# Performance work log

Hardware: AMD Instinct MI355X
Metric: run time of the kernel (lower is better)

## Reference

```python
import jax, jax.numpy as jnp
import numpy as np

N, CIN, COUT, T, V, K = 32, 64, 64, 1024, 25, 3
EPS = 1e-5  # BatchNorm2d default eps


def setup_inputs() -> dict:
    key = jax.random.key(0)
    ks = jax.random.split(key, 7)
    x = jax.random.normal(ks[0], (N, CIN, T, V), jnp.float32)
    W = jax.random.normal(ks[1], (K * COUT, CIN), jnp.float32) * 0.05  # 1x1 conv weight (squeezed)
    b = jax.random.normal(ks[2], (K * COUT,), jnp.float32) * 0.01
    A = jax.random.uniform(ks[3], (K, V, V), jnp.float32) * 0.1       # fixed adjacency buffer
    PA = jax.random.normal(ks[4], (K, V, V), jnp.float32) * 0.01      # learned adjacency offset
    gamma = jnp.ones((COUT,), jnp.float32)
    beta = jnp.zeros((COUT,), jnp.float32)
    return {"x": x, "W": W, "b": b, "A": A, "PA": PA, "gamma": gamma, "beta": beta}


def reference(x, W, b, A, PA, gamma, beta):
    n, c, t, v = x.shape
    # 1x1 conv: [n,c,t,v] x [K*COUT, c] -> [n, K*COUT, t, v]
    y = jnp.einsum('nctv,oc->notv', x, W) + b[None, :, None, None]
    y = y.reshape(n, K, COUT, t, v)
    Afull = A + PA
    # multi-subset spatial graph aggregation over joints v -> w
    agg = jnp.einsum('nkctv,kvw->nctw', y, Afull)
    # BatchNorm2d (training mode: biased batch stats over N,T,V per channel)
    mu = jnp.mean(agg, axis=(0, 2, 3), keepdims=True)
    var = jnp.var(agg, axis=(0, 2, 3), keepdims=True)
    normed = gamma[None, :, None, None] * (agg - mu) * jax.lax.rsqrt(var + EPS) + beta[None, :, None, None]
    # residual is Identity (in_channels == out_channels), then ReLU
    return jax.nn.relu(normed + x)
```

## Files before the change

### kernel.cpp

```cpp
#include <hip/hip_runtime.h>

#define N_    32
#define CIN_  64
#define COUT_ 64
#define T_    1024
#define V_    25
#define K_    3
#define TT_   4
#define EPSV  1e-5f

#define WS_BIAS2  2112
#define WS_SUM    9856
#define WS_SQ     10368
#define WS_SCALE  10880
#define WS_SHIFT  10944
#define WS_A2F    11008
#define WS_W2F    12288

typedef __attribute__((ext_vector_type(4))) float f32x4;
typedef __attribute__((ext_vector_type(8))) short short8;

__device__ __forceinline__ unsigned short f_to_bf16u(float f) {
    unsigned int b = __float_as_uint(f);
    b += 0x7fffu + ((b >> 16) & 1u);
    return (unsigned short)(b >> 16);
}

__global__ void gcn_prep(const float* __restrict__ A, const float* __restrict__ PA,
                         const float* __restrict__ b, const float* __restrict__ W,
                         float* ws) {
    __shared__ float cs[K_ * V_];
    const int tid = threadIdx.x;
    const int blk = blockIdx.x;

    if (blk == 0) {
        if (tid < K_ * V_) {
            int k = tid / V_, w = tid % V_;
            float s = 0.f;
            for (int v = 0; v < V_; ++v) {
                int idx = (k * V_ + v) * V_ + w;
                s += A[idx] + PA[idx];
            }
            cs[tid] = s;
        }
        for (int f = tid; f < 1024; f += 256) ws[WS_SUM + f] = 0.f;
        __syncthreads();
        for (int f = tid; f < COUT_ * V_; f += 256) {
            int c = f / V_, w = f - (f / V_) * V_;
            float s = 0.f;
            for (int k = 0; k < K_; ++k) s += b[k * COUT_ + c] * cs[k * V_ + w];
            ws[WS_BIAS2 + f] = s;
        }
    } else if (blk == 1) {
        unsigned short* a2 = (unsigned short*)(ws + WS_A2F);
        for (int f = tid; f < 5 * 64 * 8; f += 256) {
            int j  = f & 7;
            int l  = (f >> 3) & 63;
            int nt = f >> 9;
            int col = nt * 16 + (l & 15);
            int v   = (l >> 4) * 8 + j;
            float val = 0.f;
            if (col < 75 && v < V_) {
                int k = col / 25, w = col - (col / 25) * 25;
                int idx = (k * V_ + v) * V_ + w;
                val = A[idx] + PA[idx];
            }
            a2[f] = f_to_bf16u(val);
        }
    } else {
        unsigned short* w2 = (unsigned short*)(ws + WS_W2F);
        int lo = (blk - 2) * 6144;
        for (int f = lo + tid; f < lo + 6144; f += 256) {
            int j = f & 7;
            int l = (f >> 3) & 63;
            int g = f >> 9;
            int kci = (g % 6) * 32 + (l >> 4) * 8 + j;
            int c   = (g / 6) * 16 + (l & 15);
            int k = kci >> 6, ci = kci & 63;
            w2[f] = f_to_bf16u(W[(k * 64 + c) * 64 + ci]);
        }
    }
}

__global__ __launch_bounds__(256, 2)
void gcn_main(const float* __restrict__ x, float* __restrict__ ws,
              float* __restrict__ out) {
    __shared__ __align__(16) unsigned char smem[65280];
    unsigned short* xs16 = (unsigned short*)smem;
    unsigned short* xa16 = (unsigned short*)(smem + 20480);
    float* ostage = (float*)smem;
    float* sstat  = (float*)(smem + 25856);

    const int tid = threadIdx.x;
    const int bid = blockIdx.x;
    const int n   = bid >> 8;
    const int tc  = bid & 255;
    const int l   = tid & 63;
    const int wv  = tid >> 6;
    const int llo = l & 15;
    const int lhi = l >> 4;

    {
        unsigned int* xu = (unsigned int*)xs16;
        #pragma unroll
        for (int i = 0; i < 20; ++i) xu[i * 256 + tid] = 0u;
    }
    __syncthreads();

    const float4* xg = (const float4*)x;
    for (int f = tid; f < CIN_ * 25; f += 256) {
        int ci = f / 25;
        int j  = f - ci * 25;
        float4 g = xg[((size_t)(n * CIN_ + ci)) * 6400 + tc * 25 + j];
        int flat = 4 * j;
        int t = flat / 25;
        int v = flat - t * 25;
        float vals[4] = {g.x, g.y, g.z, g.w};
        #pragma unroll
        for (int e = 0; e < 4; ++e) {
            xs16[(ci * 4 + t) * 40 + v] = f_to_bf16u(vals[e]);
            if (++v == 25) { v = 0; ++t; }
        }
    }
    __syncthreads();

    {
        const unsigned short* a2g = (const unsigned short*)(ws + WS_A2F);
        short8 a2f[5];
        #pragma unroll
        for (int nt = 0; nt < 5; ++nt)
            a2f[nt] = *(const short8*)(a2g + (nt * 64 + l) * 8);

        #pragma unroll
        for (int q = 0; q < 4; ++q) {
            int mt = wv * 4 + q;
            short8 xf = *(const short8*)(xs16 + (mt * 16 + llo) * 40 + lhi * 8);
            f32x4 acc[5];
            #pragma unroll
            for (int nt = 0; nt < 5; ++nt) {
                f32x4 z = {0.f, 0.f, 0.f, 0.f};
                acc[nt] = __builtin_amdgcn_mfma_f32_16x16x32_bf16(xf, a2f[nt], z, 0, 0, 0);
            }
            int ci = mt * 4 + lhi;
            #pragma unroll
            for (int nt = 0; nt < 5; ++nt) {
                int col = nt * 16 + llo;
                if (col < 75) {
                    int k = (col >= 50) ? 2 : ((col >= 25) ? 1 : 0);
                    int w = col - k * 25;
                    unsigned short* dst = xa16 + w * 200 + k * 64 + ci;
                    #pragma unroll
                    for (int i = 0; i < 4; ++i)
                        dst[i * 5000] = f_to_bf16u(acc[nt][i]);
                }
            }
        }
    }
    __syncthreads();

    f32x4 c2[7];
    {
        const unsigned short* w2g = (const unsigned short*)(ws + WS_W2F);
        short8 w2f[6];
        #pragma unroll
        for (int kk = 0; kk < 6; ++kk)
            w2f[kk] = *(const short8*)(w2g + ((wv * 6 + kk) * 64 + l) * 8);

        const int c = wv * 16 + llo;
        #pragma unroll
        for (int mt = 0; mt < 7; ++mt) {
            f32x4 acc = {0.f, 0.f, 0.f, 0.f};
            #pragma unroll
            for (int kk = 0; kk < 6; ++kk) {
                short8 a = *(const short8*)(xa16 + (mt * 16 + llo) * 200 + kk * 32 + lhi * 8);
                acc = __builtin_amdgcn_mfma_f32_16x16x32_bf16(a, w2f[kk], acc, 0, 0, 0);
            }
            int rb = mt * 16 + lhi * 4;
            #pragma unroll
            for (int i = 0; i < 4; ++i) {
                int row2 = rb + i;
                if (row2 < 100) {
                    int t2 = row2 / 25;
                    int w2i = row2 - t2 * 25;
                    acc[i] += ws[WS_BIAS2 + c * 25 + w2i];
                }
            }
            c2[mt] = acc;
        }
    }
    __syncthreads();

    {
        const int c = wv * 16 + llo;
        #pragma unroll
        for (int mt = 0; mt < 7; ++mt) {
            int rb = mt * 16 + lhi * 4;
            #pragma unroll
            for (int i = 0; i < 4; ++i)
                if (rb + i < 100) ostage[c * 101 + rb + i] = c2[mt][i];
        }
    }
    __syncthreads();

    const size_t obase = ((size_t)(n * COUT_)) * 25600 + tc * 100;
    #pragma unroll 1
    for (int it = 0; it < 25; ++it) {
        int idx = it * 256 + tid;
        int cc = idx / 100;
        int r  = idx - cc * 100;
        out[obase + (size_t)cc * 25600 + r] = ostage[cc * 101 + r];
    }

    {
        int cc = tid & 63, tg = tid >> 6;
        float ls = 0.f, lq = 0.f;
        #pragma unroll
        for (int w = 0; w < 25; ++w) {
            float v = ostage[cc * 101 + tg * 25 + w];
            ls += v; lq = fmaf(v, v, lq);
        }
        sstat[(tg * 64 + cc) * 2]     = ls;
        sstat[(tg * 64 + cc) * 2 + 1] = lq;
    }
    __syncthreads();
    if (tid < 64) {
        int cc = tid;
        float s = sstat[cc * 2] + sstat[(64 + cc) * 2] + sstat[(128 + cc) * 2] + sstat[(192 + cc) * 2];
        float q = sstat[cc * 2 + 1] + sstat[(64 + cc) * 2 + 1] + sstat[(128 + cc) * 2 + 1] + sstat[(192 + cc) * 2 + 1];
        int slot = bid & 7;
        atomicAdd(&ws[WS_SUM + slot * 64 + cc], s);
        atomicAdd(&ws[WS_SQ  + slot * 64 + cc], q);
    }
}

__global__ void gcn_stats(float* ws, const float* __restrict__ gamma,
                          const float* __restrict__ beta) {
    int c = threadIdx.x;
    if (c < COUT_) {
        float s = 0.f, q = 0.f;
        #pragma unroll
        for (int slot = 0; slot < 8; ++slot) {
            s += ws[WS_SUM + slot * 64 + c];
            q += ws[WS_SQ  + slot * 64 + c];
        }
        const float cnt = (float)(N_ * T_ * V_);
        float mu  = s / cnt;
        float var = q / cnt - mu * mu;
        float rs  = rsqrtf(var + EPSV);
        float sc  = gamma[c] * rs;
        ws[WS_SCALE + c] = sc;
        ws[WS_SHIFT + c] = fmaf(-mu, sc, beta[c]);
    }
}

__global__ __launch_bounds__(256)
void gcn_finish(const float* __restrict__ x, const float* __restrict__ ws,
                float* __restrict__ out) {
    int bid = blockIdx.x;
    int c = bid & 63;
    float sc = ws[WS_SCALE + c];
    float sh = ws[WS_SHIFT + c];
    size_t base4 = (size_t)bid * 6400;
    const float4* x4 = (const float4*)x;
    float4* o4 = (float4*)out;
    #pragma unroll 2
    for (int it = 0; it < 25; ++it) {
        size_t i = base4 + it * 256 + threadIdx.x;
        float4 a  = o4[i];
        float4 xv = x4[i];
        a.x = fmaxf(0.f, fmaf(a.x, sc, sh) + xv.x);
        a.y = fmaxf(0.f, fmaf(a.y, sc, sh) + xv.y);
        a.z = fmaxf(0.f, fmaf(a.z, sc, sh) + xv.z);
        a.w = fmaxf(0.f, fmaf(a.w, sc, sh) + xv.w);
        o4[i] = a;
    }
}

extern "C" void kernel_launch(void* const* d_in, const int* in_sizes, int n_in,
                              void* d_out, int out_size, void* d_ws, size_t ws_size,
                              hipStream_t stream) {
    (void)in_sizes; (void)n_in; (void)out_size; (void)ws_size;
    const float* x     = (const float*)d_in[0];
    const float* W     = (const float*)d_in[1];
    const float* b     = (const float*)d_in[2];
    const float* A     = (const float*)d_in[3];
    const float* PA    = (const float*)d_in[4];
    const float* gamma = (const float*)d_in[5];
    const float* beta  = (const float*)d_in[6];
    float* out = (float*)d_out;
    float* ws  = (float*)d_ws;

    gcn_prep<<<4, 256, 0, stream>>>(A, PA, b, W, ws);
    gcn_main<<<N_ * (T_ / TT_), 256, 0, stream>>>(x, ws, out);
    gcn_stats<<<1, 64, 0, stream>>>(ws, gamma, beta);
    gcn_finish<<<N_ * COUT_, 256, 0, stream>>>(x, ws, out);
}
```

Before: 641.8 us.

## Halve time tile, drop LDS output staging, store and reduce stats from registers

Each block now handles 2 time steps instead of 4, which doubles the block count, cuts LDS from about 64KB to 35KB and raises launch bounds to 4 blocks per SM. The LDS staging of the output tile and the separate stats pass are removed. Outputs are written straight from MFMA accumulators to global memory, and per-channel sums are reduced with wave shuffles before the atomics. The first-stage results are packed as bf16 pairs into 8-byte LDS stores. The tradeoffs are less coalesced direct global writes, each lane storing strided rows, and twice as many atomics.

```diff
diff --git a/kernel.cpp b/kernel.cpp
--- a/kernel.cpp
+++ b/kernel.cpp
@@ -6,7 +6,7 @@
 #define T_    1024
 #define V_    25
 #define K_    3
-#define TT_   4
+#define TT_   2
 #define EPSV  1e-5f
 
 #define WS_BIAS2  2112
@@ -82,19 +82,17 @@
     }
 }
 
-__global__ __launch_bounds__(256, 2)
+__global__ __launch_bounds__(256, 4)
 void gcn_main(const float* __restrict__ x, float* __restrict__ ws,
               float* __restrict__ out) {
-    __shared__ __align__(16) unsigned char smem[65280];
+    __shared__ __align__(16) unsigned char smem[35840];
     unsigned short* xs16 = (unsigned short*)smem;
-    unsigned short* xa16 = (unsigned short*)(smem + 20480);
-    float* ostage = (float*)smem;
-    float* sstat  = (float*)(smem + 25856);
+    unsigned short* xa16 = (unsigned short*)(smem + 10240);
 
     const int tid = threadIdx.x;
     const int bid = blockIdx.x;
-    const int n   = bid >> 8;
-    const int tc  = bid & 255;
+    const int n   = bid >> 9;
+    const int tc  = bid & 511;
     const int l   = tid & 63;
     const int wv  = tid >> 6;
     const int llo = l & 15;
@@ -103,24 +101,22 @@
     {
         unsigned int* xu = (unsigned int*)xs16;
         #pragma unroll
-        for (int i = 0; i < 20; ++i) xu[i * 256 + tid] = 0u;
+        for (int i = 0; i < 10; ++i) xu[i * 256 + tid] = 0u;
     }
     __syncthreads();
 
-    const float4* xg = (const float4*)x;
+    const float2* xg = (const float2*)x;
     for (int f = tid; f < CIN_ * 25; f += 256) {
         int ci = f / 25;
         int j  = f - ci * 25;
-        float4 g = xg[((size_t)(n * CIN_ + ci)) * 6400 + tc * 25 + j];
-        int flat = 4 * j;
-        int t = flat / 25;
-        int v = flat - t * 25;
-        float vals[4] = {g.x, g.y, g.z, g.w};
-        #pragma unroll
-        for (int e = 0; e < 4; ++e) {
-            xs16[(ci * 4 + t) * 40 + v] = f_to_bf16u(vals[e]);
-            if (++v == 25) { v = 0; ++t; }
-        }
+        float2 g = xg[(size_t)(n * CIN_ + ci) * 12800 + tc * 25 + j];
+        int flat = 2 * j;
+        int t = (flat >= 25) ? 1 : 0;
+        int v = flat - 25 * t;
+        xs16[(t * 64 + ci) * 40 + v] = f_to_bf16u(g.x);
+        int v2 = v + 1, t2 = t;
+        if (v2 == 25) { v2 = 0; t2 = 1; }
+        xs16[(t2 * 64 + ci) * 40 + v2] = f_to_bf16u(g.y);
     }
     __syncthreads();
 
@@ -132,33 +128,32 @@
             a2f[nt] = *(const short8*)(a2g + (nt * 64 + l) * 8);
 
         #pragma unroll
-        for (int q = 0; q < 4; ++q) {
-            int mt = wv * 4 + q;
+        for (int q = 0; q < 2; ++q) {
+            int mt = wv * 2 + q;
             short8 xf = *(const short8*)(xs16 + (mt * 16 + llo) * 40 + lhi * 8);
-            f32x4 acc[5];
+            int rb = mt * 16 + lhi * 4;
+            int t  = rb >> 6;
+            int ci = rb & 63;
             #pragma unroll
             for (int nt = 0; nt < 5; ++nt) {
                 f32x4 z = {0.f, 0.f, 0.f, 0.f};
-                acc[nt] = __builtin_amdgcn_mfma_f32_16x16x32_bf16(xf, a2f[nt], z, 0, 0, 0);
-            }
-            int ci = mt * 4 + lhi;
-            #pragma unroll
-            for (int nt = 0; nt < 5; ++nt) {
+                f32x4 acc = __builtin_amdgcn_mfma_f32_16x16x32_bf16(xf, a2f[nt], z, 0, 0, 0);
                 int col = nt * 16 + llo;
                 if (col < 75) {
                     int k = (col >= 50) ? 2 : ((col >= 25) ? 1 : 0);
                     int w = col - k * 25;
-                    unsigned short* dst = xa16 + w * 200 + k * 64 + ci;
-                    #pragma unroll
-                    for (int i = 0; i < 4; ++i)
-                        dst[i * 5000] = f_to_bf16u(acc[nt][i]);
+                    unsigned int lo = (unsigned int)f_to_bf16u(acc[0]) |
+                                      ((unsigned int)f_to_bf16u(acc[1]) << 16);
+                    unsigned int hi = (unsigned int)f_to_bf16u(acc[2]) |
+                                      ((unsigned int)f_to_bf16u(acc[3]) << 16);
+                    uint2 pk; pk.x = lo; pk.y = hi;
+                    *(uint2*)(xa16 + (t * 25 + w) * 200 + k * 64 + ci) = pk;
                 }
             }
         }
     }
     __syncthreads();
 
-    f32x4 c2[7];
     {
         const unsigned short* w2g = (const unsigned short*)(ws + WS_W2F);
         short8 w2f[6];
@@ -167,69 +162,40 @@
             w2f[kk] = *(const short8*)(w2g + ((wv * 6 + kk) * 64 + l) * 8);
 
         const int c = wv * 16 + llo;
-        #pragma unroll
-        for (int mt = 0; mt < 7; ++mt) {
+        const size_t obase = ((size_t)(n * COUT_ + c)) * 25600 + (size_t)tc * 50;
+        float lsum = 0.f, lsq = 0.f;
+
+        #pragma unroll
+        for (int mt = 0; mt < 4; ++mt) {
             f32x4 acc = {0.f, 0.f, 0.f, 0.f};
             #pragma unroll
             for (int kk = 0; kk < 6; ++kk) {
                 short8 a = *(const short8*)(xa16 + (mt * 16 + llo) * 200 + kk * 32 + lhi * 8);
                 acc = __builtin_amdgcn_mfma_f32_16x16x32_bf16(a, w2f[kk], acc, 0, 0, 0);
             }
-            int rb = mt * 16 + lhi * 4;
+            int rbase = mt * 16 + lhi * 4;
             #pragma unroll
             for (int i = 0; i < 4; ++i) {
-                int row2 = rb + i;
-                if (row2 < 100) {
-                    int t2 = row2 / 25;
-                    int w2i = row2 - t2 * 25;
-                    acc[i] += ws[WS_BIAS2 + c * 25 + w2i];
+                int r = rbase + i;
+                if (r < 50) {
+                    int t2 = (r >= 25) ? 1 : 0;
+                    int w2 = r - 25 * t2;
+                    float v = acc[i] + ws[WS_BIAS2 + c * 25 + w2];
+                    out[obase + r] = v;
+                    lsum += v;
+                    lsq = fmaf(v, v, lsq);
                 }
             }
-            c2[mt] = acc;
-        }
-    }
-    __syncthreads();
-
-    {
-        const int c = wv * 16 + llo;
-        #pragma unroll
-        for (int mt = 0; mt < 7; ++mt) {
-            int rb = mt * 16 + lhi * 4;
-            #pragma unroll
-            for (int i = 0; i < 4; ++i)
-                if (rb + i < 100) ostage[c * 101 + rb + i] = c2[mt][i];
-        }
-    }
-    __syncthreads();
-
-    const size_t obase = ((size_t)(n * COUT_)) * 25600 + tc * 100;
-    #pragma unroll 1
-    for (int it = 0; it < 25; ++it) {
-        int idx = it * 256 + tid;
-        int cc = idx / 100;
-        int r  = idx - cc * 100;
-        out[obase + (size_t)cc * 25600 + r] = ostage[cc * 101 + r];
-    }
-
-    {
-        int cc = tid & 63, tg = tid >> 6;
-        float ls = 0.f, lq = 0.f;
-        #pragma unroll
-        for (int w = 0; w < 25; ++w) {
-            float v = ostage[cc * 101 + tg * 25 + w];
-            ls += v; lq = fmaf(v, v, lq);
-        }
-        sstat[(tg * 64 + cc) * 2]     = ls;
-        sstat[(tg * 64 + cc) * 2 + 1] = lq;
-    }
-    __syncthreads();
-    if (tid < 64) {
-        int cc = tid;
-        float s = sstat[cc * 2] + sstat[(64 + cc) * 2] + sstat[(128 + cc) * 2] + sstat[(192 + cc) * 2];
-        float q = sstat[cc * 2 + 1] + sstat[(64 + cc) * 2 + 1] + sstat[(128 + cc) * 2 + 1] + sstat[(192 + cc) * 2 + 1];
-        int slot = bid & 7;
-        atomicAdd(&ws[WS_SUM + slot * 64 + cc], s);
-        atomicAdd(&ws[WS_SQ  + slot * 64 + cc], q);
+        }
+        lsum += __shfl_xor(lsum, 16);
+        lsum += __shfl_xor(lsum, 32);
+        lsq  += __shfl_xor(lsq, 16);
+        lsq  += __shfl_xor(lsq, 32);
+        if (l < 16) {
+            int slot = bid & 7;
+            atomicAdd(&ws[WS_SUM + slot * 64 + c], lsum);
+            atomicAdd(&ws[WS_SQ  + slot * 64 + c], lsq);
+        }
     }
 }
 
```

Result: no change. 647.2 us (+0.8%).
